# Kernel optimization log

Hardware: AMD Instinct MI355X
Metric: run time of the kernel (lower is better)

Reference implementation:

```python
import jax, jax.numpy as jnp
import numpy as np

L, B = 512, 1
NODE_DIM, EDGE_DIM = 256, 128
MLP_DIM = NODE_DIM + EDGE_DIM  # 384 ('concat' outer op)
LN_EPS = 1e-5


def setup_inputs() -> dict:
    key = jax.random.key(0)
    ks = jax.random.split(key, 12)
    s = 0.02
    return {
        "x": jax.random.normal(ks[0], (L, B, NODE_DIM), dtype=jnp.float32),
        "z": jax.random.normal(ks[1], (B, L, L, EDGE_DIM), dtype=jnp.float32),
        "Wd": jax.random.normal(ks[2], (NODE_DIM // 2, NODE_DIM), dtype=jnp.float32) * s,
        "bd": jnp.zeros((NODE_DIM // 2,), dtype=jnp.float32),
        "W1": jax.random.normal(ks[3], (MLP_DIM, MLP_DIM), dtype=jnp.float32) * s,
        "b1": jnp.zeros((MLP_DIM,), dtype=jnp.float32),
        "W2": jax.random.normal(ks[4], (MLP_DIM, MLP_DIM), dtype=jnp.float32) * s,
        "b2": jnp.zeros((MLP_DIM,), dtype=jnp.float32),
        "Wo": jax.random.normal(ks[5], (EDGE_DIM, MLP_DIM), dtype=jnp.float32) * s,
        "bo": jnp.zeros((EDGE_DIM,), dtype=jnp.float32),
        "gamma": jnp.ones((EDGE_DIM,), dtype=jnp.float32),
        "beta": jnp.zeros((EDGE_DIM,), dtype=jnp.float32),
    }


def reference(x, z, Wd, bd, W1, b1, W2, b2, Wo, bo, gamma, beta):
    # down-project nodes: x [L,B,nd] -> x_down [B,L,nd//2]
    x_down = jnp.swapaxes(x @ Wd.T + bd, 0, 1)
    n = x_down.shape[1]
    # outer 'concat': edge_bias [B,L,L,nd]
    row = jnp.broadcast_to(x_down[:, :, None, :], (x_down.shape[0], n, n, x_down.shape[-1]))
    col = jnp.broadcast_to(x_down[:, None, :, :], (x_down.shape[0], n, n, x_down.shape[-1]))
    edge_bias = jnp.concatenate([row, col], axis=-1)
    z_in = jnp.concatenate([edge_bias, z], axis=-1)  # [B,L,L,MLP_DIM]
    # edge MLP (Linear-ReLU-Linear-ReLU) + residual, then out linear
    h = jax.nn.relu(z_in @ W1.T + b1)
    h = jax.nn.relu(h @ W2.T + b2)
    out = (h + z_in) @ Wo.T + bo  # [B,L,L,EDGE_DIM]
    # LayerNorm over last dim
    mu = out.mean(axis=-1, keepdims=True)
    var = out.var(axis=-1, keepdims=True)
    return (out - mu) * jax.lax.rsqrt(var + LN_EPS) * gamma + beta
```

## Files before the change

kernel.cpp:

```cpp
#include <hip/hip_runtime.h>


using bf16x8 = __attribute__((ext_vector_type(8))) __bf16;
using f32x16 = __attribute__((ext_vector_type(16))) float;

#define LPAD 392
#define OPAD 132

__device__ inline unsigned short f2bf(float f) {
    union { float f; unsigned int u; } v; v.f = f;
    unsigned int r = v.u + 0x7fffu + ((v.u >> 16) & 1u);
    return (unsigned short)(r >> 16);
}
__device__ inline float bf2f(unsigned short h) {
    union { unsigned int u; float f; } v; v.u = ((unsigned int)h) << 16;
    return v.f;
}

__global__ void k_xdown(const float* __restrict__ x, const float* __restrict__ Wd,
                        const float* __restrict__ bd, unsigned short* __restrict__ xd) {
    __shared__ float sx[8 * 256];
    const int t = threadIdx.x;
    const int ibase = blockIdx.x * 8;
    for (int c = t; c < 8 * 256; c += 128) sx[c] = x[ibase * 256 + c];
    __syncthreads();
    const float bias = bd[t];
    const float* wr = &Wd[t * 256];
    for (int ii = 0; ii < 8; ++ii) {
        const float* xr = &sx[ii * 256];
        float sum = 0.f;
#pragma unroll 8
        for (int k = 0; k < 256; k += 4) {
            float4 wv = *(const float4*)&wr[k];
            float4 xv = *(const float4*)&xr[k];
            sum += wv.x * xv.x + wv.y * xv.y + wv.z * xv.z + wv.w * xv.w;
        }
        xd[(ibase + ii) * 128 + t] = f2bf(sum + bias);
    }
}

__global__ void k_wswz(const float* __restrict__ W, unsigned short* __restrict__ dst, int total) {
    int c = blockIdx.x * 256 + threadIdx.x;
    if (c >= total) return;
    int lane = c & 63;
    int ks = (c >> 6) % 24;
    int nt = c / (24 * 64);
    int n = nt * 32 + (lane & 31);
    int k0 = ks * 16 + ((lane >> 5) << 3);
    const float* src = &W[n * 384 + k0];
    unsigned short tmp[8];
#pragma unroll
    for (int j = 0; j < 8; ++j) tmp[j] = f2bf(src[j]);
    *(uint4*)&dst[(size_t)c * 8] = *(const uint4*)tmp;
}

__global__ __launch_bounds__(768) void edge_main(
    const float* __restrict__ z, const unsigned short* __restrict__ xd,
    const unsigned short* __restrict__ W1s, const unsigned short* __restrict__ W2s,
    const unsigned short* __restrict__ Wos,
    const float* __restrict__ b1, const float* __restrict__ b2,
    const float* __restrict__ bo, const float* __restrict__ gamma,
    const float* __restrict__ beta, float* __restrict__ out)
{
    extern __shared__ char smem[];
    unsigned short* sA = (unsigned short*)smem;
    unsigned short* sH = (unsigned short*)(smem + 64 * LPAD * 2);
    float* sO = (float*)sH;

    const int tid = threadIdx.x;
    const int lane = tid & 63;
    const int w = tid >> 6;
    const int i = blockIdx.x >> 3;
    const int j0 = (blockIdx.x & 7) << 6;

    for (int c = tid; c < 64 * 16; c += 768) {
        int r = c >> 4, cc = (c & 15) << 3;
        *(uint4*)&sA[r * LPAD + cc] = *(const uint4*)&xd[i * 128 + cc];
        *(uint4*)&sA[r * LPAD + 128 + cc] = *(const uint4*)&xd[(j0 + r) * 128 + cc];
    }
    for (int c = tid; c < 64 * 32; c += 768) {
        int r = c >> 5, cc = (c & 31) << 2;
        float4 v = *(const float4*)&z[((size_t)((i << 9) + j0 + r) << 7) + cc];
        ushort4 o;
        o.x = f2bf(v.x); o.y = f2bf(v.y); o.z = f2bf(v.z); o.w = f2bf(v.w);
        *(ushort4*)&sA[r * LPAD + 256 + cc] = o;
    }
    __syncthreads();

    const int arow = lane & 31;
    const int kof = (lane >> 5) << 3;
    const int half2 = (lane >> 5) << 2;

    {
        f32x16 acc0 = {}, acc1 = {};
#pragma unroll 2
        for (int ks = 0; ks < 24; ++ks) {
            int k = ks * 16 + kof;
            bf16x8 a0 = *(const bf16x8*)&sA[arow * LPAD + k];
            bf16x8 a1 = *(const bf16x8*)&sA[(arow + 32) * LPAD + k];
            bf16x8 b = *(const bf16x8*)&W1s[(size_t)((w * 24 + ks) * 64 + lane) * 8];
            acc0 = __builtin_amdgcn_mfma_f32_32x32x16_bf16(a0, b, acc0, 0, 0, 0);
            acc1 = __builtin_amdgcn_mfma_f32_32x32x16_bf16(a1, b, acc1, 0, 0, 0);
        }
        int col = w * 32 + arow;
        float bias = b1[col];
#pragma unroll
        for (int rg = 0; rg < 16; ++rg) {
            int rr = half2 + (rg & 3) + ((rg >> 2) << 3);
            float v0 = acc0[rg] + bias; v0 = v0 > 0.f ? v0 : 0.f;
            float v1 = acc1[rg] + bias; v1 = v1 > 0.f ? v1 : 0.f;
            sH[rr * LPAD + col] = f2bf(v0);
            sH[(rr + 32) * LPAD + col] = f2bf(v1);
        }
    }
    __syncthreads();

    {
        f32x16 acc0 = {}, acc1 = {};
#pragma unroll 2
        for (int ks = 0; ks < 24; ++ks) {
            int k = ks * 16 + kof;
            bf16x8 a0 = *(const bf16x8*)&sH[arow * LPAD + k];
            bf16x8 a1 = *(const bf16x8*)&sH[(arow + 32) * LPAD + k];
            bf16x8 b = *(const bf16x8*)&W2s[(size_t)((w * 24 + ks) * 64 + lane) * 8];
            acc0 = __builtin_amdgcn_mfma_f32_32x32x16_bf16(a0, b, acc0, 0, 0, 0);
            acc1 = __builtin_amdgcn_mfma_f32_32x32x16_bf16(a1, b, acc1, 0, 0, 0);
        }
        int col = w * 32 + arow;
        float bias = b2[col];
#pragma unroll
        for (int rg = 0; rg < 16; ++rg) {
            int rr = half2 + (rg & 3) + ((rg >> 2) << 3);
            float v0 = acc0[rg] + bias; v0 = v0 > 0.f ? v0 : 0.f;
            float v1 = acc1[rg] + bias; v1 = v1 > 0.f ? v1 : 0.f;
            float r0 = bf2f(sA[rr * LPAD + col]);
            float r1 = bf2f(sA[(rr + 32) * LPAD + col]);
            sA[rr * LPAD + col] = f2bf(v0 + r0);
            sA[(rr + 32) * LPAD + col] = f2bf(v1 + r1);
        }
    }
    __syncthreads();

    if (w < 8) {
        const int mt3 = w >> 2;
        const int nt3 = w & 3;
        f32x16 acc = {};
#pragma unroll 2
        for (int ks = 0; ks < 24; ++ks) {
            int k = ks * 16 + kof;
            bf16x8 a0 = *(const bf16x8*)&sA[(arow + mt3 * 32) * LPAD + k];
            bf16x8 b = *(const bf16x8*)&Wos[(size_t)((nt3 * 24 + ks) * 64 + lane) * 8];
            acc = __builtin_amdgcn_mfma_f32_32x32x16_bf16(a0, b, acc, 0, 0, 0);
        }
        int col = nt3 * 32 + arow;
        float bias = bo[col];
#pragma unroll
        for (int rg = 0; rg < 16; ++rg) {
            int rr = mt3 * 32 + half2 + (rg & 3) + ((rg >> 2) << 3);
            sO[rr * OPAD + col] = acc[rg] + bias;
        }
    }
    __syncthreads();

    if (tid < 256) {
        const int r = tid >> 2;
        const int q = tid & 3;
        float s = 0.f, ss = 0.f;
#pragma unroll
        for (int ii = 0; ii < 32; ++ii) {
            float v = sO[r * OPAD + q + (ii << 2)];
            s += v; ss += v * v;
        }
        s += __shfl_xor(s, 1);  ss += __shfl_xor(ss, 1);
        s += __shfl_xor(s, 2);  ss += __shfl_xor(ss, 2);
        const float mean = s * (1.f / 128.f);
        const float var = ss * (1.f / 128.f) - mean * mean;
        const float rstd = rsqrtf(var + 1e-5f);
        float* po = &out[((size_t)((i << 9) + j0 + r)) << 7];
#pragma unroll
        for (int ii = 0; ii < 8; ++ii) {
            int c0 = q * 32 + (ii << 2);
            float4 v = *(const float4*)&sO[r * OPAD + c0];
            float4 g = *(const float4*)&gamma[c0];
            float4 bb = *(const float4*)&beta[c0];
            float4 o;
            o.x = (v.x - mean) * rstd * g.x + bb.x;
            o.y = (v.y - mean) * rstd * g.y + bb.y;
            o.z = (v.z - mean) * rstd * g.z + bb.z;
            o.w = (v.w - mean) * rstd * g.w + bb.w;
            *(float4*)&po[c0] = o;
        }
    }
}

extern "C" void kernel_launch(void* const* d_in, const int* in_sizes, int n_in,
                              void* d_out, int out_size, void* d_ws, size_t ws_size,
                              hipStream_t stream) {
    const float* x     = (const float*)d_in[0];
    const float* z     = (const float*)d_in[1];
    const float* Wd    = (const float*)d_in[2];
    const float* bd    = (const float*)d_in[3];
    const float* W1    = (const float*)d_in[4];
    const float* b1    = (const float*)d_in[5];
    const float* W2    = (const float*)d_in[6];
    const float* b2    = (const float*)d_in[7];
    const float* Wo    = (const float*)d_in[8];
    const float* bo    = (const float*)d_in[9];
    const float* gamma = (const float*)d_in[10];
    const float* beta  = (const float*)d_in[11];
    float* out = (float*)d_out;

    unsigned short* xd  = (unsigned short*)d_ws;
    unsigned short* W1s = (unsigned short*)((char*)d_ws + 131072);
    unsigned short* W2s = (unsigned short*)((char*)d_ws + 425984);
    unsigned short* Wos = (unsigned short*)((char*)d_ws + 720896);

    hipLaunchKernelGGL(k_xdown, dim3(64), dim3(128), 0, stream, x, Wd, bd, xd);
    hipLaunchKernelGGL(k_wswz, dim3(72), dim3(256), 0, stream, W1, W1s, 12 * 24 * 64);
    hipLaunchKernelGGL(k_wswz, dim3(72), dim3(256), 0, stream, W2, W2s, 12 * 24 * 64);
    hipLaunchKernelGGL(k_wswz, dim3(24), dim3(256), 0, stream, Wo, Wos, 4 * 24 * 64);

    const size_t smem = (size_t)(64 * LPAD * 2) * 2;
    hipLaunchKernelGGL(edge_main, dim3(4096), dim3(768), smem, stream,
                       z, xd, W1s, W2s, Wos, b1, b2, bo, gamma, beta, out);
}
```

Baseline: 553.7 us.

## Prefetch GEMM weight fragments into registers ahead of each stage barrier

Each stage's weight fragments (24 bf16x8 per lane) are now loaded into registers before the preceding sync, and the MFMA loops are fully unrolled. This overlaps global weight fetches with the z/xd staging and with the previous stage's epilogue, taking global loads out of the inner MFMA loops. It also adds a launch-bounds occupancy hint of 3 and splits k_xdown into one block per row. The cost is higher register pressure: 96 VGPRs of prefetched weights plus accumulators at 768 threads could cause spilling or lower occupancy.

```diff
diff --git a/kernel.cpp b/kernel.cpp
--- a/kernel.cpp
+++ b/kernel.cpp
@@ -19,24 +19,20 @@
 
 __global__ void k_xdown(const float* __restrict__ x, const float* __restrict__ Wd,
                         const float* __restrict__ bd, unsigned short* __restrict__ xd) {
-    __shared__ float sx[8 * 256];
+    __shared__ float sx[256];
     const int t = threadIdx.x;
-    const int ibase = blockIdx.x * 8;
-    for (int c = t; c < 8 * 256; c += 128) sx[c] = x[ibase * 256 + c];
-    __syncthreads();
-    const float bias = bd[t];
+    const int i = blockIdx.x;
+    if (t < 64) *(float4*)&sx[t * 4] = *(const float4*)&x[i * 256 + t * 4];
+    __syncthreads();
     const float* wr = &Wd[t * 256];
-    for (int ii = 0; ii < 8; ++ii) {
-        const float* xr = &sx[ii * 256];
-        float sum = 0.f;
+    float sum = 0.f;
 #pragma unroll 8
-        for (int k = 0; k < 256; k += 4) {
-            float4 wv = *(const float4*)&wr[k];
-            float4 xv = *(const float4*)&xr[k];
-            sum += wv.x * xv.x + wv.y * xv.y + wv.z * xv.z + wv.w * xv.w;
-        }
-        xd[(ibase + ii) * 128 + t] = f2bf(sum + bias);
-    }
+    for (int k = 0; k < 256; k += 4) {
+        float4 wv = *(const float4*)&wr[k];
+        float4 xv = *(const float4*)&sx[k];
+        sum += wv.x * xv.x + wv.y * xv.y + wv.z * xv.z + wv.w * xv.w;
+    }
+    xd[i * 128 + t] = f2bf(sum + bd[t]);
 }
 
 __global__ void k_wswz(const float* __restrict__ W, unsigned short* __restrict__ dst, int total) {
@@ -54,7 +50,7 @@
     *(uint4*)&dst[(size_t)c * 8] = *(const uint4*)tmp;
 }
 
-__global__ __launch_bounds__(768) void edge_main(
+__global__ __launch_bounds__(768, 3) void edge_main(
     const float* __restrict__ z, const unsigned short* __restrict__ xd,
     const unsigned short* __restrict__ W1s, const unsigned short* __restrict__ W2s,
     const unsigned short* __restrict__ Wos,
@@ -73,6 +69,15 @@
     const int i = blockIdx.x >> 3;
     const int j0 = (blockIdx.x & 7) << 6;
 
+    const int arow = lane & 31;
+    const int kof = (lane >> 5) << 3;
+    const int half2 = (lane >> 5) << 2;
+
+    bf16x8 b1f[24];
+#pragma unroll
+    for (int ks = 0; ks < 24; ++ks)
+        b1f[ks] = *(const bf16x8*)&W1s[(size_t)((w * 24 + ks) * 64 + lane) * 8];
+
     for (int c = tid; c < 64 * 16; c += 768) {
         int r = c >> 4, cc = (c & 15) << 3;
         *(uint4*)&sA[r * LPAD + cc] = *(const uint4*)&xd[i * 128 + cc];
@@ -87,20 +92,15 @@
     }
     __syncthreads();
 
-    const int arow = lane & 31;
-    const int kof = (lane >> 5) << 3;
-    const int half2 = (lane >> 5) << 2;
-
     {
         f32x16 acc0 = {}, acc1 = {};
-#pragma unroll 2
+#pragma unroll
         for (int ks = 0; ks < 24; ++ks) {
             int k = ks * 16 + kof;
             bf16x8 a0 = *(const bf16x8*)&sA[arow * LPAD + k];
             bf16x8 a1 = *(const bf16x8*)&sA[(arow + 32) * LPAD + k];
-            bf16x8 b = *(const bf16x8*)&W1s[(size_t)((w * 24 + ks) * 64 + lane) * 8];
-            acc0 = __builtin_amdgcn_mfma_f32_32x32x16_bf16(a0, b, acc0, 0, 0, 0);
-            acc1 = __builtin_amdgcn_mfma_f32_32x32x16_bf16(a1, b, acc1, 0, 0, 0);
+            acc0 = __builtin_amdgcn_mfma_f32_32x32x16_bf16(a0, b1f[ks], acc0, 0, 0, 0);
+            acc1 = __builtin_amdgcn_mfma_f32_32x32x16_bf16(a1, b1f[ks], acc1, 0, 0, 0);
         }
         int col = w * 32 + arow;
         float bias = b1[col];
@@ -113,18 +113,22 @@
             sH[(rr + 32) * LPAD + col] = f2bf(v1);
         }
     }
+
+    bf16x8 b2f[24];
+#pragma unroll
+    for (int ks = 0; ks < 24; ++ks)
+        b2f[ks] = *(const bf16x8*)&W2s[(size_t)((w * 24 + ks) * 64 + lane) * 8];
     __syncthreads();
 
     {
         f32x16 acc0 = {}, acc1 = {};
-#pragma unroll 2
+#pragma unroll
         for (int ks = 0; ks < 24; ++ks) {
             int k = ks * 16 + kof;
             bf16x8 a0 = *(const bf16x8*)&sH[arow * LPAD + k];
             bf16x8 a1 = *(const bf16x8*)&sH[(arow + 32) * LPAD + k];
-            bf16x8 b = *(const bf16x8*)&W2s[(size_t)((w * 24 + ks) * 64 + lane) * 8];
-            acc0 = __builtin_amdgcn_mfma_f32_32x32x16_bf16(a0, b, acc0, 0, 0, 0);
-            acc1 = __builtin_amdgcn_mfma_f32_32x32x16_bf16(a1, b, acc1, 0, 0, 0);
+            acc0 = __builtin_amdgcn_mfma_f32_32x32x16_bf16(a0, b2f[ks], acc0, 0, 0, 0);
+            acc1 = __builtin_amdgcn_mfma_f32_32x32x16_bf16(a1, b2f[ks], acc1, 0, 0, 0);
         }
         int col = w * 32 + arow;
         float bias = b2[col];
@@ -139,19 +143,26 @@
             sA[(rr + 32) * LPAD + col] = f2bf(v1 + r1);
         }
     }
+
+    bf16x8 bof[24];
+    if (w < 8) {
+        const int nt3 = w & 3;
+#pragma unroll
+        for (int ks = 0; ks < 24; ++ks)
+            bof[ks] = *(const bf16x8*)&Wos[(size_t)((nt3 * 24 + ks) * 64 + lane) * 8];
+    }
     __syncthreads();
 
     if (w < 8) {
         const int mt3 = w >> 2;
-        const int nt3 = w & 3;
         f32x16 acc = {};
-#pragma unroll 2
+#pragma unroll
         for (int ks = 0; ks < 24; ++ks) {
             int k = ks * 16 + kof;
             bf16x8 a0 = *(const bf16x8*)&sA[(arow + mt3 * 32) * LPAD + k];
-            bf16x8 b = *(const bf16x8*)&Wos[(size_t)((nt3 * 24 + ks) * 64 + lane) * 8];
-            acc = __builtin_amdgcn_mfma_f32_32x32x16_bf16(a0, b, acc, 0, 0, 0);
-        }
+            acc = __builtin_amdgcn_mfma_f32_32x32x16_bf16(a0, bof[ks], acc, 0, 0, 0);
+        }
+        const int nt3 = w & 3;
         int col = nt3 * 32 + arow;
         float bias = bo[col];
 #pragma unroll
@@ -215,7 +226,7 @@
     unsigned short* W2s = (unsigned short*)((char*)d_ws + 425984);
     unsigned short* Wos = (unsigned short*)((char*)d_ws + 720896);
 
-    hipLaunchKernelGGL(k_xdown, dim3(64), dim3(128), 0, stream, x, Wd, bd, xd);
+    hipLaunchKernelGGL(k_xdown, dim3(512), dim3(128), 0, stream, x, Wd, bd, xd);
     hipLaunchKernelGGL(k_wswz, dim3(72), dim3(256), 0, stream, W1, W1s, 12 * 24 * 64);
     hipLaunchKernelGGL(k_wswz, dim3(72), dim3(256), 0, stream, W2, W2s, 12 * 24 * 64);
     hipLaunchKernelGGL(k_wswz, dim3(24), dim3(256), 0, stream, Wo, Wos, 4 * 24 * 64);
```

Result: no change. 555.5 us (+0.3%).
